# Performance work log

Hardware: AMD Instinct MI355X
Metric: run time of the kernel (lower is better)

## Reference

```python
import jax, jax.numpy as jnp
import numpy as np

N_NODES = 100000
N_EDGES = 1600000
IN_CH, HID_CH, OUT_CH = 128, 128, 64


def setup_inputs() -> dict:
    key = jax.random.key(0)
    k1, k2, k3, k4 = jax.random.split(key, 4)
    x = jax.random.normal(k1, (N_NODES, IN_CH), dtype=jnp.float32)
    edge_index = jax.random.randint(k2, (2, N_EDGES), 0, N_NODES, dtype=jnp.int32)
    # Glorot-style init for GCNConv linear weights, zeros for bias (PyG default)
    s1 = (6.0 / (IN_CH + HID_CH)) ** 0.5
    s2 = (6.0 / (HID_CH + OUT_CH)) ** 0.5
    W1 = jax.random.uniform(k3, (IN_CH, HID_CH), jnp.float32, -s1, s1)
    W2 = jax.random.uniform(k4, (HID_CH, OUT_CH), jnp.float32, -s2, s2)
    b1 = jnp.zeros((HID_CH,), jnp.float32)
    b2 = jnp.zeros((OUT_CH,), jnp.float32)
    return {"x": x, "edge_index": edge_index, "W1": W1, "b1": b1, "W2": W2, "b2": b2}


def reference(x, edge_index, W1, b1, W2, b2):
    N = x.shape[0]
    # gcn_norm with add_self_loops=True, edge_weight=None -> ones
    loop = jnp.arange(N, dtype=edge_index.dtype)
    row = jnp.concatenate([edge_index[0], loop])  # source nodes
    col = jnp.concatenate([edge_index[1], loop])  # target nodes
    ew = jnp.ones(row.shape[0], dtype=x.dtype)
    deg = jax.ops.segment_sum(ew, col, num_segments=N)           # in-degree incl. self-loops
    dis = jnp.where(deg > 0, jax.lax.rsqrt(deg), 0.0)            # deg^{-1/2}, inf -> 0
    norm = dis[row] * ew * dis[col]                              # per-edge normalization

    def gcn_conv(h, W, b):
        h = h @ W                                                # [N, d_out]
        msg = h[row] * norm[:, None]                             # gather + scale [E+N, d_out]
        return jax.ops.segment_sum(msg, col, num_segments=N) + b  # scatter-add

    h = jax.nn.relu(gcn_conv(x, W1, b1))
    # F.dropout with training=False is identity (eval mode reference)
    return gcn_conv(h, W2, b2)
```

## Files before the change

kernel.cpp:

```cpp
#include <hip/hip_runtime.h>
#include <hip/hip_fp16.h>
#include <type_traits>


constexpr int BSH = 9;
constexpr int BNODES = 1 << BSH;
constexpr int CHUNK = 4096;
constexpr int CAP = 12288;

typedef __attribute__((ext_vector_type(8))) _Float16 half8;
typedef __attribute__((ext_vector_type(4))) float f32x4;

__global__ __launch_bounds__(256) void zero_kernel(int* __restrict__ p, int n) {
    int i = blockIdx.x * 256 + threadIdx.x;
    if (i < n) p[i] = 0;
}

__global__ __launch_bounds__(256) void zero_halfs_kernel(__half* __restrict__ p, int n) {
    int i = threadIdx.x;
    if (i < n) reinterpret_cast<unsigned short*>(p)[i] = 0;
}

__global__ __launch_bounds__(256) void hist_kernel(const int* __restrict__ col,
                                                   int* __restrict__ bhist,
                                                   int E, int NB) {
    __shared__ int lh[256];
    int t = threadIdx.x;
    lh[t] = 0;
    __syncthreads();
    for (int i = blockIdx.x * 256 + t; i < E; i += gridDim.x * 256)
        atomicAdd(&lh[col[i] >> BSH], 1);
    __syncthreads();
    if (t < NB && lh[t]) atomicAdd(&bhist[t], lh[t]);
}

__global__ __launch_bounds__(256) void bbase_scan_kernel(const int* __restrict__ bhist,
                                                         int* __restrict__ bbase,
                                                         int* __restrict__ bcur, int NB) {
    __shared__ int s[256];
    int t = threadIdx.x;
    int v = (t < NB) ? bhist[t] : 0;
    s[t] = v;
    __syncthreads();
    for (int d = 1; d < 256; d <<= 1) {
        int u = (t >= d) ? s[t - d] : 0;
        __syncthreads();
        s[t] += u;
        __syncthreads();
    }
    if (t < NB) { bbase[t] = s[t] - v; bcur[t] = s[t] - v; }
    if (t == NB - 1) bbase[NB] = s[t];
}

__global__ __launch_bounds__(256) void bucket_scatter_kernel(const int* __restrict__ row,
                                                             const int* __restrict__ col,
                                                             int* __restrict__ bcur,
                                                             int2* __restrict__ pairs,
                                                             int E, int NB) {
    __shared__ int2 sp[CHUNK];
    __shared__ int lhist[256], lofs[256], lcur[256], gbase[256];
    int t = threadIdx.x;
    int start = blockIdx.x * CHUNK;
    int cnt = min(CHUNK, E - start);
    lhist[t] = 0;
    __syncthreads();
    for (int i = t; i < cnt; i += 256)
        atomicAdd(&lhist[col[start + i] >> BSH], 1);
    __syncthreads();
    int v = lhist[t];
    lofs[t] = v;
    __syncthreads();
    for (int d = 1; d < 256; d <<= 1) {
        int u = (t >= d) ? lofs[t - d] : 0;
        __syncthreads();
        lofs[t] += u;
        __syncthreads();
    }
    int excl = lofs[t] - v;
    lofs[t] = excl;
    lcur[t] = excl;
    if (t < NB && v > 0) gbase[t] = atomicAdd(&bcur[t], v);
    __syncthreads();
    for (int i = t; i < cnt; i += 256) {
        int c = col[start + i];
        int s = row[start + i];
        int lp = atomicAdd(&lcur[c >> BSH], 1);
        sp[lp] = make_int2(s, c);
    }
    __syncthreads();
    for (int i = t; i < cnt; i += 256) {
        int2 pr = sp[i];
        int b = pr.y >> BSH;
        pairs[gbase[b] + (i - lofs[b])] = pr;
    }
}

__global__ __launch_bounds__(256) void place_kernel(const int2* __restrict__ pairs,
                                                    const int* __restrict__ bbase,
                                                    int* __restrict__ off,
                                                    float* __restrict__ dis,
                                                    int* __restrict__ csr, int N, int NB) {
    __shared__ int lhist[BNODES], lexcl[BNODES], lcur2[BNODES];
    __shared__ int sscan[256];
    __shared__ int lout[CAP];
    int b = blockIdx.x;
    int t = threadIdx.x;
    int n0 = b << BSH;
    int n1 = min(n0 + BNODES, N);
    int nn = n1 - n0;
    int base = bbase[b];
    int cnt = bbase[b + 1] - base;
    lhist[2 * t] = 0;
    lhist[2 * t + 1] = 0;
    __syncthreads();
    for (int i = t; i < cnt; i += 256)
        atomicAdd(&lhist[pairs[base + i].y - n0], 1);
    __syncthreads();
    int a0 = lhist[2 * t], a1 = lhist[2 * t + 1];
    int ps = a0 + a1;
    sscan[t] = ps;
    __syncthreads();
    for (int d = 1; d < 256; d <<= 1) {
        int u = (t >= d) ? sscan[t - d] : 0;
        __syncthreads();
        sscan[t] += u;
        __syncthreads();
    }
    int pexcl = sscan[t] - ps;
    lexcl[2 * t] = pexcl;
    lexcl[2 * t + 1] = pexcl + a0;
    lcur2[2 * t] = pexcl;
    lcur2[2 * t + 1] = pexcl + a0;
    __syncthreads();
    for (int i = t; i < nn; i += 256) {
        off[n0 + i] = base + lexcl[i];
        dis[n0 + i] = rsqrtf((float)(lhist[i] + 1));
    }
    if (b == NB - 1 && t == 0) off[N] = base + cnt;
    for (int i = t; i < cnt; i += 256) {
        int2 pr = pairs[base + i];
        int lp = atomicAdd(&lcur2[pr.y - n0], 1);
        if (lp < CAP) lout[lp] = pr.x;
        else csr[base + lp] = pr.x;
    }
    __syncthreads();
    int staged = min(cnt, CAP);
    for (int i = t; i < staged; i += 256) csr[base + i] = lout[i];
}

template<int TN>
__global__ __launch_bounds__(256) void wtrans_kernel(const float* __restrict__ W,
                                                     _Float16* __restrict__ WT) {
    int i = blockIdx.x * 256 + threadIdx.x;
    if (i < TN * 128) {
        int n = i % TN, k = i / TN;
        WT[n * 128 + k] = (_Float16)W[k * TN + n];
    }
}

template<int TN, typename TI>
__global__ __launch_bounds__(256) void gemm_kernel(const TI* __restrict__ X,
                                                   const _Float16* __restrict__ WT,
                                                   const float* __restrict__ dis,
                                                   __half* __restrict__ Y, int M) {
    constexpr int K = 128;
    constexpr int NT = TN / 16;
    constexpr int LDA = 136;
    __shared__ _Float16 Ah[64 * LDA];
    __shared__ _Float16 Bh[TN * LDA];
    int tid = threadIdx.x;
    int row0 = blockIdx.x * 64;

#pragma unroll
    for (int j = 0; j < TN / 16; ++j) {
        int lin = tid + j * 256;
        int n = lin >> 4, kq = lin & 15;
        *(uint4*)&Bh[n * LDA + kq * 8] = *(const uint4*)(WT + n * 128 + kq * 8);
    }
    if constexpr (std::is_same<TI, float>::value) {
#pragma unroll
        for (int j = 0; j < 8; ++j) {
            int lin = tid + j * 256;
            int r = lin >> 5, kq = lin & 31;
            int row = row0 + r;
            float4 v = make_float4(0.f, 0.f, 0.f, 0.f);
            if (row < M) v = *(const float4*)(X + (size_t)row * K + kq * 4);
            __half2 h01 = __float22half2_rn(make_float2(v.x, v.y));
            __half2 h23 = __float22half2_rn(make_float2(v.z, v.w));
            uint2 u = make_uint2(*reinterpret_cast<unsigned*>(&h01),
                                 *reinterpret_cast<unsigned*>(&h23));
            *(uint2*)&Ah[r * LDA + kq * 4] = u;
        }
    } else {
#pragma unroll
        for (int j = 0; j < 4; ++j) {
            int lin = tid + j * 256;
            int r = lin >> 4, kq = lin & 15;
            int row = row0 + r;
            uint4 u = make_uint4(0, 0, 0, 0);
            if (row < M) u = *(const uint4*)(X + (size_t)row * K + kq * 8);
            *(uint4*)&Ah[r * LDA + kq * 8] = u;
        }
    }
    __syncthreads();

    int w = tid >> 6, l = tid & 63;
    int lr = l & 15, kg = l >> 4;
    f32x4 acc[NT];
#pragma unroll
    for (int nt = 0; nt < NT; ++nt) acc[nt] = (f32x4){0.f, 0.f, 0.f, 0.f};

    const _Float16* arow = &Ah[(w * 16 + lr) * LDA + kg * 8];
#pragma unroll
    for (int ks = 0; ks < 4; ++ks) {
        half8 af = *(const half8*)(arow + ks * 32);
#pragma unroll
        for (int nt = 0; nt < NT; ++nt) {
            half8 bf = *(const half8*)(&Bh[(nt * 16 + lr) * LDA + ks * 32 + kg * 8]);
            acc[nt] = __builtin_amdgcn_mfma_f32_16x16x32_f16(af, bf, acc[nt], 0, 0, 0);
        }
    }

#pragma unroll
    for (int j = 0; j < 4; ++j) {
        int grow = row0 + w * 16 + kg * 4 + j;
        if (grow < M) {
            float sc = dis[grow];
#pragma unroll
            for (int nt = 0; nt < NT; ++nt)
                Y[(size_t)grow * TN + nt * 16 + lr] = __float2half_rn(sc * acc[nt][j]);
        }
    }
}

template<int C, bool RELU, typename TOUT>
__global__ __launch_bounds__(256) void agg_kernel(const __half* __restrict__ Hs,
                                                  const int* __restrict__ off,
                                                  const int* __restrict__ src,
                                                  const float* __restrict__ dis,
                                                  const float* __restrict__ bias,
                                                  TOUT* __restrict__ out, int N) {
    constexpr int HPL = C / 16;
    constexpr int NV = HPL / 2;
    using VT = std::conditional_t<HPL == 8, uint4, uint2>;
    int node = blockIdx.x * 16 + (threadIdx.x >> 4);
    if (node >= N) return;
    int lane = threadIdx.x & 15;
    const __half* hbase = Hs + lane * HPL;
    float dv = dis[node];
    float acc[HPL];
    {
        VT sv = *(const VT*)(hbase + (size_t)node * C);
        const unsigned int* u = reinterpret_cast<const unsigned int*>(&sv);
#pragma unroll
        for (int q = 0; q < NV; ++q) {
            float2 f = __half22float2(*reinterpret_cast<const __half2*>(&u[q]));
            acc[2 * q] = f.x;
            acc[2 * q + 1] = f.y;
        }
    }
    int e0 = off[node], e1 = off[node + 1];
    for (int e = e0; e < e1; e += 8) {
        int s[8];
#pragma unroll
        for (int k = 0; k < 8; ++k) {
            int idx = e + k;
            s[k] = (idx < e1) ? src[idx] : N;
        }
        VT v[8];
#pragma unroll
        for (int k = 0; k < 8; ++k)
            v[k] = *(const VT*)(hbase + (size_t)s[k] * C);
#pragma unroll
        for (int k = 0; k < 8; ++k) {
            const unsigned int* u = reinterpret_cast<const unsigned int*>(&v[k]);
#pragma unroll
            for (int q = 0; q < NV; ++q) {
                float2 f = __half22float2(*reinterpret_cast<const __half2*>(&u[q]));
                acc[2 * q] += f.x;
                acc[2 * q + 1] += f.y;
            }
        }
    }
    float r[HPL];
#pragma unroll
    for (int f = 0; f < HPL; ++f) {
        r[f] = fmaf(dv, acc[f], bias[lane * HPL + f]);
        if (RELU) r[f] = fmaxf(r[f], 0.0f);
    }
    if constexpr (std::is_same<TOUT, __half>::value) {
        __half2 hv[NV];
#pragma unroll
        for (int q = 0; q < NV; ++q)
            hv[q] = __float22half2_rn(make_float2(r[2 * q], r[2 * q + 1]));
        *(VT*)(out + (size_t)node * C + lane * HPL) = *reinterpret_cast<VT*>(&hv[0]);
    } else {
        if constexpr (HPL == 8) {
            *(float4*)(out + (size_t)node * C + lane * 8) =
                make_float4(r[0], r[1], r[2], r[3]);
            *(float4*)(out + (size_t)node * C + lane * 8 + 4) =
                make_float4(r[4], r[5], r[6], r[7]);
        } else {
            *(float4*)(out + (size_t)node * C + lane * 4) =
                make_float4(r[0], r[1], r[2], r[3]);
        }
    }
}

extern "C" void kernel_launch(void* const* d_in, const int* in_sizes, int n_in,
                              void* d_out, int out_size, void* d_ws, size_t ws_size,
                              hipStream_t stream) {
    const float* x  = (const float*)d_in[0];
    const int*   ei = (const int*)d_in[1];
    const float* W1 = (const float*)d_in[2];
    const float* b1 = (const float*)d_in[3];
    const float* W2 = (const float*)d_in[4];
    const float* b2 = (const float*)d_in[5];
    float* out = (float*)d_out;

    int N = in_sizes[0] / 128;
    int E = in_sizes[1] / 2;
    const int* row = ei;
    const int* col = ei + E;
    int NB = (N + BNODES - 1) >> BSH;

    char* ws = (char*)d_ws;
    size_t o = 0;
    auto alloc = [&](size_t bytes) -> void* {
        void* p = ws + o;
        o = (o + bytes + 255) & ~(size_t)255;
        return p;
    };
    int*      bhist = (int*)alloc((size_t)(NB + 1) * 4);
    int*      bbase = (int*)alloc((size_t)(NB + 1) * 4);
    int*      bcur  = (int*)alloc((size_t)NB * 4);
    int*      off   = (int*)alloc((size_t)(N + 1) * 4);
    float*    dis   = (float*)alloc((size_t)N * 4);
    int*      csr   = (int*)alloc((size_t)E * 4);
    _Float16* w1t   = (_Float16*)alloc(128 * 128 * 2);
    _Float16* w2t   = (_Float16*)alloc(64 * 128 * 2);
    __half*   xw    = (__half*)alloc(((size_t)N * 128 + 128) * 2);
    __half*   h     = (__half*)alloc(((size_t)N * 128 + 128) * 2);
    int2*     pairs = (int2*)alloc((size_t)E * 8);
    __half*   hw2   = xw;

    zero_kernel<<<1, 256, 0, stream>>>(bhist, NB);
    wtrans_kernel<128><<<64, 256, 0, stream>>>(W1, w1t);
    wtrans_kernel<64><<<32, 256, 0, stream>>>(W2, w2t);
    hist_kernel<<<1024, 256, 0, stream>>>(col, bhist, E, NB);
    bbase_scan_kernel<<<1, 256, 0, stream>>>(bhist, bbase, bcur, NB);
    bucket_scatter_kernel<<<(E + CHUNK - 1) / CHUNK, 256, 0, stream>>>(row, col, bcur,
                                                                       pairs, E, NB);
    place_kernel<<<NB, 256, 0, stream>>>(pairs, bbase, off, dis, csr, N, NB);

    gemm_kernel<128, float><<<(N + 63) / 64, 256, 0, stream>>>(x, w1t, dis, xw, N);
    zero_halfs_kernel<<<1, 256, 0, stream>>>(xw + (size_t)N * 128, 128);
    agg_kernel<128, true, __half><<<(N + 15) / 16, 256, 0, stream>>>(xw, off, csr, dis,
                                                                     b1, h, N);
    gemm_kernel<64, __half><<<(N + 63) / 64, 256, 0, stream>>>(h, w2t, dis, hw2, N);
    zero_halfs_kernel<<<1, 256, 0, stream>>>(hw2 + (size_t)N * 64, 64);
    agg_kernel<64, false, float><<<(N + 15) / 16, 256, 0, stream>>>(hw2, off, csr, dis,
                                                                    b2, out, N);
}
```

Baseline: 204.3 us.

## Pad per-node CSR neighbor lists to multiples of eight for vector index loads

The CSR build now pads each node's neighbor list to a multiple of eight, filling the padding with the zero sentinel row N, and stores padded degrees in a new array. The aggregation kernel reads indices as two aligned int4 loads with no bounds checks, using only the padded count. The 64-channel aggregation also switches to 8 lanes per node with 16-byte loads, so each block covers 32 nodes. The cost is extra padded gathers of the sentinel row and more CSR storage plus fill work. Correctness depends on the padded total fitting inside the per-bucket PADSTRIDE slack.

```diff
diff --git a/kernel.cpp b/kernel.cpp
--- a/kernel.cpp
+++ b/kernel.cpp
@@ -6,7 +6,8 @@
 constexpr int BSH = 9;
 constexpr int BNODES = 1 << BSH;
 constexpr int CHUNK = 4096;
-constexpr int CAP = 12288;
+constexpr int CAP = 13312;
+constexpr int PADSTRIDE = 3592;
 
 typedef __attribute__((ext_vector_type(8))) _Float16 half8;
 typedef __attribute__((ext_vector_type(4))) float f32x4;
@@ -98,6 +99,7 @@
 __global__ __launch_bounds__(256) void place_kernel(const int2* __restrict__ pairs,
                                                     const int* __restrict__ bbase,
                                                     int* __restrict__ off,
+                                                    int* __restrict__ pd,
                                                     float* __restrict__ dis,
                                                     int* __restrict__ csr, int N, int NB) {
     __shared__ int lhist[BNODES], lexcl[BNODES], lcur2[BNODES];
@@ -110,6 +112,7 @@
     int nn = n1 - n0;
     int base = bbase[b];
     int cnt = bbase[b + 1] - base;
+    int base_pad = ((base + 7) & ~7) + PADSTRIDE * b;
     lhist[2 * t] = 0;
     lhist[2 * t + 1] = 0;
     __syncthreads();
@@ -117,7 +120,8 @@
         atomicAdd(&lhist[pairs[base + i].y - n0], 1);
     __syncthreads();
     int a0 = lhist[2 * t], a1 = lhist[2 * t + 1];
-    int ps = a0 + a1;
+    int a0p = (a0 + 7) & ~7, a1p = (a1 + 7) & ~7;
+    int ps = a0p + a1p;
     sscan[t] = ps;
     __syncthreads();
     for (int d = 1; d < 256; d <<= 1) {
@@ -128,24 +132,28 @@
     }
     int pexcl = sscan[t] - ps;
     lexcl[2 * t] = pexcl;
-    lexcl[2 * t + 1] = pexcl + a0;
+    lexcl[2 * t + 1] = pexcl + a0p;
     lcur2[2 * t] = pexcl;
-    lcur2[2 * t + 1] = pexcl + a0;
-    __syncthreads();
+    lcur2[2 * t + 1] = pexcl + a0p;
+    __syncthreads();
+    int padded_total = sscan[255];
     for (int i = t; i < nn; i += 256) {
-        off[n0 + i] = base + lexcl[i];
+        off[n0 + i] = base_pad + lexcl[i];
+        pd[n0 + i] = (lhist[i] + 7) & ~7;
         dis[n0 + i] = rsqrtf((float)(lhist[i] + 1));
     }
-    if (b == NB - 1 && t == 0) off[N] = base + cnt;
+    int staged = min(padded_total, CAP);
+    for (int i = t; i < staged; i += 256) lout[i] = N;
+    for (int i = CAP + t; i < padded_total; i += 256) csr[base_pad + i] = N;
+    __syncthreads();
     for (int i = t; i < cnt; i += 256) {
         int2 pr = pairs[base + i];
         int lp = atomicAdd(&lcur2[pr.y - n0], 1);
         if (lp < CAP) lout[lp] = pr.x;
-        else csr[base + lp] = pr.x;
-    }
-    __syncthreads();
-    int staged = min(cnt, CAP);
-    for (int i = t; i < staged; i += 256) csr[base + i] = lout[i];
+        else csr[base_pad + lp] = pr.x;
+    }
+    __syncthreads();
+    for (int i = t; i < staged; i += 256) csr[base_pad + i] = lout[i];
 }
 
 template<int TN>
@@ -236,74 +244,67 @@
 template<int C, bool RELU, typename TOUT>
 __global__ __launch_bounds__(256) void agg_kernel(const __half* __restrict__ Hs,
                                                   const int* __restrict__ off,
+                                                  const int* __restrict__ pd,
                                                   const int* __restrict__ src,
                                                   const float* __restrict__ dis,
                                                   const float* __restrict__ bias,
                                                   TOUT* __restrict__ out, int N) {
-    constexpr int HPL = C / 16;
-    constexpr int NV = HPL / 2;
-    using VT = std::conditional_t<HPL == 8, uint4, uint2>;
-    int node = blockIdx.x * 16 + (threadIdx.x >> 4);
+    constexpr int L = C / 8;
+    constexpr int NPB = 256 / L;
+    int node = blockIdx.x * NPB + threadIdx.x / L;
     if (node >= N) return;
-    int lane = threadIdx.x & 15;
-    const __half* hbase = Hs + lane * HPL;
+    int lane = threadIdx.x & (L - 1);
+    const __half* hbase = Hs + lane * 8;
     float dv = dis[node];
-    float acc[HPL];
+    float acc[8];
     {
-        VT sv = *(const VT*)(hbase + (size_t)node * C);
-        const unsigned int* u = reinterpret_cast<const unsigned int*>(&sv);
-#pragma unroll
-        for (int q = 0; q < NV; ++q) {
+        uint4 sv = *(const uint4*)(hbase + (size_t)node * C);
+        const unsigned* u = reinterpret_cast<const unsigned*>(&sv);
+#pragma unroll
+        for (int q = 0; q < 4; ++q) {
             float2 f = __half22float2(*reinterpret_cast<const __half2*>(&u[q]));
             acc[2 * q] = f.x;
             acc[2 * q + 1] = f.y;
         }
     }
-    int e0 = off[node], e1 = off[node + 1];
-    for (int e = e0; e < e1; e += 8) {
-        int s[8];
+    int e = off[node];
+    int nb = pd[node] >> 3;
+    for (int b = 0; b < nb; ++b, e += 8) {
+        int4 sa = *(const int4*)(src + e);
+        int4 sb = *(const int4*)(src + e + 4);
+        int s[8] = {sa.x, sa.y, sa.z, sa.w, sb.x, sb.y, sb.z, sb.w};
+        uint4 v[8];
+#pragma unroll
+        for (int k = 0; k < 8; ++k)
+            v[k] = *(const uint4*)(hbase + (size_t)s[k] * C);
 #pragma unroll
         for (int k = 0; k < 8; ++k) {
-            int idx = e + k;
-            s[k] = (idx < e1) ? src[idx] : N;
-        }
-        VT v[8];
-#pragma unroll
-        for (int k = 0; k < 8; ++k)
-            v[k] = *(const VT*)(hbase + (size_t)s[k] * C);
-#pragma unroll
-        for (int k = 0; k < 8; ++k) {
-            const unsigned int* u = reinterpret_cast<const unsigned int*>(&v[k]);
-#pragma unroll
-            for (int q = 0; q < NV; ++q) {
+            const unsigned* u = reinterpret_cast<const unsigned*>(&v[k]);
+#pragma unroll
+            for (int q = 0; q < 4; ++q) {
                 float2 f = __half22float2(*reinterpret_cast<const __half2*>(&u[q]));
                 acc[2 * q] += f.x;
                 acc[2 * q + 1] += f.y;
             }
         }
     }
-    float r[HPL];
-#pragma unroll
-    for (int f = 0; f < HPL; ++f) {
-        r[f] = fmaf(dv, acc[f], bias[lane * HPL + f]);
+    float r[8];
+#pragma unroll
+    for (int f = 0; f < 8; ++f) {
+        r[f] = fmaf(dv, acc[f], bias[lane * 8 + f]);
         if (RELU) r[f] = fmaxf(r[f], 0.0f);
     }
     if constexpr (std::is_same<TOUT, __half>::value) {
-        __half2 hv[NV];
-#pragma unroll
-        for (int q = 0; q < NV; ++q)
+        __half2 hv[4];
+#pragma unroll
+        for (int q = 0; q < 4; ++q)
             hv[q] = __float22half2_rn(make_float2(r[2 * q], r[2 * q + 1]));
-        *(VT*)(out + (size_t)node * C + lane * HPL) = *reinterpret_cast<VT*>(&hv[0]);
+        *(uint4*)(out + (size_t)node * C + lane * 8) = *reinterpret_cast<uint4*>(&hv[0]);
     } else {
-        if constexpr (HPL == 8) {
-            *(float4*)(out + (size_t)node * C + lane * 8) =
-                make_float4(r[0], r[1], r[2], r[3]);
-            *(float4*)(out + (size_t)node * C + lane * 8 + 4) =
-                make_float4(r[4], r[5], r[6], r[7]);
-        } else {
-            *(float4*)(out + (size_t)node * C + lane * 4) =
-                make_float4(r[0], r[1], r[2], r[3]);
-        }
+        *(float4*)(out + (size_t)node * C + lane * 8) =
+            make_float4(r[0], r[1], r[2], r[3]);
+        *(float4*)(out + (size_t)node * C + lane * 8 + 4) =
+            make_float4(r[4], r[5], r[6], r[7]);
     }
 }
 
@@ -335,8 +336,9 @@
     int*      bbase = (int*)alloc((size_t)(NB + 1) * 4);
     int*      bcur  = (int*)alloc((size_t)NB * 4);
     int*      off   = (int*)alloc((size_t)(N + 1) * 4);
+    int*      pd    = (int*)alloc((size_t)N * 4);
     float*    dis   = (float*)alloc((size_t)N * 4);
-    int*      csr   = (int*)alloc((size_t)E * 4);
+    int*      csr   = (int*)alloc(((size_t)E + (size_t)PADSTRIDE * NB + 16) * 4);
     _Float16* w1t   = (_Float16*)alloc(128 * 128 * 2);
     _Float16* w2t   = (_Float16*)alloc(64 * 128 * 2);
     __half*   xw    = (__half*)alloc(((size_t)N * 128 + 128) * 2);
@@ -351,14 +353,14 @@
     bbase_scan_kernel<<<1, 256, 0, stream>>>(bhist, bbase, bcur, NB);
     bucket_scatter_kernel<<<(E + CHUNK - 1) / CHUNK, 256, 0, stream>>>(row, col, bcur,
                                                                        pairs, E, NB);
-    place_kernel<<<NB, 256, 0, stream>>>(pairs, bbase, off, dis, csr, N, NB);
+    place_kernel<<<NB, 256, 0, stream>>>(pairs, bbase, off, pd, dis, csr, N, NB);
 
     gemm_kernel<128, float><<<(N + 63) / 64, 256, 0, stream>>>(x, w1t, dis, xw, N);
     zero_halfs_kernel<<<1, 256, 0, stream>>>(xw + (size_t)N * 128, 128);
-    agg_kernel<128, true, __half><<<(N + 15) / 16, 256, 0, stream>>>(xw, off, csr, dis,
-                                                                     b1, h, N);
+    agg_kernel<128, true, __half><<<(N + 15) / 16, 256, 0, stream>>>(xw, off, pd, csr,
+                                                                     dis, b1, h, N);
     gemm_kernel<64, __half><<<(N + 63) / 64, 256, 0, stream>>>(h, w2t, dis, hw2, N);
     zero_halfs_kernel<<<1, 256, 0, stream>>>(hw2 + (size_t)N * 64, 64);
-    agg_kernel<64, false, float><<<(N + 15) / 16, 256, 0, stream>>>(hw2, off, csr, dis,
-                                                                    b2, out, N);
-}
+    agg_kernel<64, false, float><<<(N + 31) / 32, 256, 0, stream>>>(hw2, off, pd, csr,
+                                                                    dis, b2, out, N);
+}
```

Result: no change. 205.1 us (+0.4%).
